# Kernel tuning notes

Measured on AMD Instinct MI355X. Metric: run time of the kernel, lower is better.

Reference implementation:

```python
import jax, jax.numpy as jnp
import numpy as np

INPUT_DIM, HIDDEN_DIM, OUTPUT_DIM = 512, 1024, 512
BATCH, SEQ = 64, 512


def setup_inputs() -> dict:
    key = jax.random.key(0)
    ks = jax.random.split(key, 7)
    s_ih = 1.0 / np.sqrt(HIDDEN_DIM)
    x = jax.random.normal(ks[0], (BATCH, SEQ, INPUT_DIM), dtype=jnp.float32)
    W_ih = jax.random.uniform(ks[1], (HIDDEN_DIM, INPUT_DIM), jnp.float32, -s_ih, s_ih)
    W_hh = jax.random.uniform(ks[2], (HIDDEN_DIM, HIDDEN_DIM), jnp.float32, -s_ih, s_ih)
    b_ih = jax.random.uniform(ks[3], (HIDDEN_DIM,), jnp.float32, -s_ih, s_ih)
    b_hh = jax.random.uniform(ks[4], (HIDDEN_DIM,), jnp.float32, -s_ih, s_ih)
    s_fc = 1.0 / np.sqrt(HIDDEN_DIM)
    W_fc = jax.random.uniform(ks[5], (OUTPUT_DIM, HIDDEN_DIM), jnp.float32, -s_fc, s_fc)
    b_fc = jax.random.uniform(ks[6], (OUTPUT_DIM,), jnp.float32, -s_fc, s_fc)
    return {"x": x, "W_ih": W_ih, "W_hh": W_hh, "b_ih": b_ih,
            "b_hh": b_hh, "W_fc": W_fc, "b_fc": b_fc}


def reference(x, W_ih, W_hh, b_ih, b_hh, W_fc, b_fc):
    B = x.shape[0]
    # Precompute input projections for all timesteps in one big GEMM: [S, B, H]
    xp = jnp.einsum('bsi,hi->sbh', x, W_ih) + b_ih + b_hh

    def step(h, xp_t):
        h_new = jnp.tanh(xp_t + h @ W_hh.T)
        return h_new, None

    h0 = jnp.zeros((B, W_hh.shape[0]), dtype=x.dtype)
    h_final, _ = jax.lax.scan(step, h0, xp)
    return h_final @ W_fc.T + b_fc
```

## Files before the change

kernel.cpp:

```cpp
#include <hip/hip_runtime.h>
#include <hip/hip_fp16.h>

typedef _Float16 f16;
typedef _Float16 half8 __attribute__((ext_vector_type(8)));
typedef _Float16 half4 __attribute__((ext_vector_type(4)));
typedef float f32x4_t __attribute__((ext_vector_type(4)));
typedef unsigned int uint;
typedef unsigned int uint32x4 __attribute__((ext_vector_type(4)));

#define IN_DIM 512
#define H_DIM 1024
#define OUT_DIM 512
#define NBATCH 64
#define NSEQ 512
#define NGROUP 4
#define MB 16
#define WPG 16
#define NJ 64

__global__ __launch_bounds__(256) void cvt_f32_f16_k(const float* __restrict__ src,
                                                     f16* __restrict__ dst, int n) {
  int i = (blockIdx.x * 256 + threadIdx.x) * 4;
  if (i + 3 < n) {
    float4 v = *(const float4*)(src + i);
    half4 h;
    h[0] = (f16)v.x; h[1] = (f16)v.y; h[2] = (f16)v.z; h[3] = (f16)v.w;
    *(half4*)(dst + i) = h;
  }
}

__global__ __launch_bounds__(256) void bias_sum_k(const float* __restrict__ a,
                                                  const float* __restrict__ b,
                                                  float* __restrict__ o) {
  int i = blockIdx.x * 256 + threadIdx.x;
  if (i < H_DIM) o[i] = a[i] + b[i];
}

__global__ __launch_bounds__(256) void xp_gemm_k(
    const float* __restrict__ x, const float* __restrict__ wih,
    const float* __restrict__ bsum, f16* __restrict__ xp2)
{
  __shared__ f16 Alds[128 * 32];
  __shared__ f16 Blds[128 * 32];
  const int tid = threadIdx.x;
  const int l = tid & 63;
  const int w = tid >> 6;
  const int r0 = blockIdx.x * 128;
  const int n0 = blockIdx.y * 128;
  const int wm = (w >> 1) << 6;
  const int wn = (w & 1) << 6;
  const int srow = tid >> 1;
  const int scol = (tid & 1) << 4;
  const float* ax = x   + (size_t)(r0 + srow) * IN_DIM + scol;
  const float* bw = wih + (size_t)(n0 + srow) * IN_DIM + scol;
  const uint swz  = (uint)(srow & 7) << 4;
  const uint soff = (uint)srow * 64 + (uint)(tid & 1) * 32;
  char* Ab = (char*)Alds;
  char* Bb = (char*)Blds;

  f32x4_t acc[4][4];
  f32x4_t zv; zv[0] = 0.f; zv[1] = 0.f; zv[2] = 0.f; zv[3] = 0.f;
#pragma unroll
  for (int i = 0; i < 4; ++i)
#pragma unroll
    for (int j = 0; j < 4; ++j) acc[i][j] = zv;

  for (int k0 = 0; k0 < IN_DIM; k0 += 32) {
    float4 a0 = *(const float4*)(ax + k0);
    float4 a1 = *(const float4*)(ax + k0 + 4);
    float4 a2 = *(const float4*)(ax + k0 + 8);
    float4 a3 = *(const float4*)(ax + k0 + 12);
    float4 c0 = *(const float4*)(bw + k0);
    float4 c1 = *(const float4*)(bw + k0 + 4);
    float4 c2 = *(const float4*)(bw + k0 + 8);
    float4 c3 = *(const float4*)(bw + k0 + 12);
    __syncthreads();
    half8 pa0, pa1, pb0, pb1;
    pa0[0]=(f16)a0.x; pa0[1]=(f16)a0.y; pa0[2]=(f16)a0.z; pa0[3]=(f16)a0.w;
    pa0[4]=(f16)a1.x; pa0[5]=(f16)a1.y; pa0[6]=(f16)a1.z; pa0[7]=(f16)a1.w;
    pa1[0]=(f16)a2.x; pa1[1]=(f16)a2.y; pa1[2]=(f16)a2.z; pa1[3]=(f16)a2.w;
    pa1[4]=(f16)a3.x; pa1[5]=(f16)a3.y; pa1[6]=(f16)a3.z; pa1[7]=(f16)a3.w;
    pb0[0]=(f16)c0.x; pb0[1]=(f16)c0.y; pb0[2]=(f16)c0.z; pb0[3]=(f16)c0.w;
    pb0[4]=(f16)c1.x; pb0[5]=(f16)c1.y; pb0[6]=(f16)c1.z; pb0[7]=(f16)c1.w;
    pb1[0]=(f16)c2.x; pb1[1]=(f16)c2.y; pb1[2]=(f16)c2.z; pb1[3]=(f16)c2.w;
    pb1[4]=(f16)c3.x; pb1[5]=(f16)c3.y; pb1[6]=(f16)c3.z; pb1[7]=(f16)c3.w;
    *(half8*)(Ab + (soff ^ swz)) = pa0;
    *(half8*)(Ab + ((soff + 16) ^ swz)) = pa1;
    *(half8*)(Bb + (soff ^ swz)) = pb0;
    *(half8*)(Bb + ((soff + 16) ^ swz)) = pb1;
    __syncthreads();
    half8 af[4], bf[4];
#pragma unroll
    for (int mt = 0; mt < 4; ++mt) {
      uint rr = (uint)(wm + mt * 16 + (l & 15));
      uint off = rr * 64 + ((uint)(l >> 4) << 4);
      af[mt] = *(const half8*)(Ab + (off ^ ((rr & 7) << 4)));
    }
#pragma unroll
    for (int nt = 0; nt < 4; ++nt) {
      uint rr = (uint)(wn + nt * 16 + (l & 15));
      uint off = rr * 64 + ((uint)(l >> 4) << 4);
      bf[nt] = *(const half8*)(Bb + (off ^ ((rr & 7) << 4)));
    }
#pragma unroll
    for (int mt = 0; mt < 4; ++mt)
#pragma unroll
      for (int nt = 0; nt < 4; ++nt)
        acc[mt][nt] = __builtin_amdgcn_mfma_f32_16x16x32_f16(af[mt], bf[nt], acc[mt][nt], 0, 0, 0);
  }

#pragma unroll
  for (int nt = 0; nt < 4; ++nt) {
    const int n = n0 + wn + nt * 16 + (l & 15);
    const float bv = bsum[n];
#pragma unroll
    for (int mt = 0; mt < 4; ++mt) {
#pragma unroll
      for (int i = 0; i < 4; ++i) {
        int r = r0 + wm + mt * 16 + ((l >> 4) << 2) + i;
        int s = r & (NSEQ - 1);
        int b = r >> 9;
        xp2[((size_t)s * NBATCH + b) * H_DIM + n] = (f16)(acc[mt][nt][i] + bv);
      }
    }
  }
}

__global__ __launch_bounds__(256) void rnn_scan_k(
    const f16* __restrict__ whh2, const f16* __restrict__ xp2,
    f16* __restrict__ hbuf, uint* __restrict__ flags)
{
  __shared__ f16 hlds[MB * H_DIM];
  const int tid = threadIdx.x;
  const int l   = tid & 63;
  const int w   = tid >> 6;
  const int bid = blockIdx.x;
  const int xcd = bid & 7;
  const int g    = xcd >> 1;
  const int slot = ((bid >> 3) << 1) | (xcd & 1);
  const int j0   = slot * NJ + w * 16;
  const int c     = l & 15;
  const int brow0 = (l >> 4) << 2;

  half8 wf[32];
  {
    const f16* wp = whh2 + (size_t)(j0 + c) * H_DIM + ((l >> 4) << 3);
#pragma unroll
    for (int kt = 0; kt < 32; ++kt) wf[kt] = *(const half8*)(wp + kt * 32);
  }

  f16* hb0 = hbuf + (size_t)g * (2 * MB * H_DIM);
  uint* gflags = flags + g * 64;
  const int myflag = slot * 4 + w;
  const uint roff = (uint)c * 2048 + ((uint)(l >> 4) << 4);
  const uint rswz = ((uint)c & 7) << 4;
  char* hldsc = (char*)hlds;

  for (int t = 0; t < NSEQ; ++t) {
    const f16* hcur = hb0 + (t & 1) * (MB * H_DIM);
    uint* hnxt32 = (uint*)(hb0 + ((t + 1) & 1) * (MB * H_DIM));

    const f16* xpb = xp2 + ((size_t)t * NBATCH + g * MB + brow0) * H_DIM + (j0 + c);
    f16 x0 = xpb[0];
    f16 x1 = xpb[H_DIM];
    f16 x2 = xpb[2 * H_DIM];
    f16 x3 = xpb[3 * H_DIM];

    f32x4_t acc;
    acc[0] = (float)x0; acc[1] = (float)x1; acc[2] = (float)x2; acc[3] = (float)x3;

    if (t > 0) {
      if (w == 0) {
        while (true) {
          uint v = __hip_atomic_load(&gflags[l], __ATOMIC_RELAXED, __HIP_MEMORY_SCOPE_AGENT);
          if (__all((int)(v >= (uint)t))) break;
        }
      }
      __syncthreads();

      uint32x4 sv[8];
#pragma unroll
      for (int q = 0; q < 8; ++q) {
        const char* p = (const char*)hcur + (size_t)(q * 256 + tid) * 16;
        asm volatile("global_load_dwordx4 %0, %1, off sc0 sc1"
                     : "=v"(sv[q]) : "v"(p) : "memory");
      }
      asm volatile("s_waitcnt vmcnt(0)" ::: "memory");
      __builtin_amdgcn_sched_barrier(0);
#pragma unroll
      for (int q = 0; q < 8; ++q) {
        uint boff = (uint)(q * 256 + tid) * 16;
        uint row = boff >> 11;
        *(uint32x4*)(hldsc + (boff ^ ((row & 7) << 4))) = sv[q];
      }
      __syncthreads();

#pragma unroll
      for (int kt = 0; kt < 32; ++kt) {
        half8 af = *(const half8*)(hldsc + ((roff + (uint)kt * 64) ^ rswz));
        acc = __builtin_amdgcn_mfma_f32_16x16x32_f16(af, wf[kt], acc, 0, 0, 0);
      }
    }

    uint st[4];
#pragma unroll
    for (int i = 0; i < 4; ++i) {
      float pre = acc[i];
      float e = __expf(2.0f * pre);
      float th = 1.0f - 2.0f / (e + 1.0f);
      f16 hf = (f16)th;
      uint myv = (uint)__builtin_bit_cast(unsigned short, hf);
      uint pv = __shfl_xor(myv, 1, 64);
      st[i] = myv | (pv << 16);
    }
    if ((c & 1) == 0) {
#pragma unroll
      for (int i = 0; i < 4; ++i) {
        uint idx = (uint)(brow0 + i) * 512 + (uint)((j0 + c) >> 1);
        __hip_atomic_store(hnxt32 + idx, st[i], __ATOMIC_RELAXED, __HIP_MEMORY_SCOPE_AGENT);
      }
    }
    asm volatile("s_waitcnt vmcnt(0)" ::: "memory");
    if (l == 0) {
      __hip_atomic_store(&gflags[myflag], (uint)(t + 1), __ATOMIC_RELAXED, __HIP_MEMORY_SCOPE_AGENT);
    }
  }
}

__global__ __launch_bounds__(64) void fc_out_k(
    const f16* __restrict__ hbuf, const f16* __restrict__ wfc2,
    const float* __restrict__ bfc, float* __restrict__ out)
{
  const int l = threadIdx.x;
  const int wg = blockIdx.x;
  const int m0 = wg & 3;
  const int n0 = (wg >> 2) << 4;
  const f16* ap = hbuf + (size_t)m0 * (2 * MB * H_DIM)
                  + (size_t)(l & 15) * H_DIM + ((l >> 4) << 3);
  const f16* bp = wfc2 + (size_t)(n0 + (l & 15)) * H_DIM + ((l >> 4) << 3);
  f32x4_t acc;
  float bv = bfc[n0 + (l & 15)];
  acc[0] = bv; acc[1] = bv; acc[2] = bv; acc[3] = bv;
#pragma unroll
  for (int kt = 0; kt < 32; ++kt) {
    half8 a = *(const half8*)(ap + kt * 32);
    half8 b = *(const half8*)(bp + kt * 32);
    acc = __builtin_amdgcn_mfma_f32_16x16x32_f16(a, b, acc, 0, 0, 0);
  }
  const int b0 = (m0 << 4) + ((l >> 4) << 2);
  const int o  = n0 + (l & 15);
#pragma unroll
  for (int i = 0; i < 4; ++i) out[(size_t)(b0 + i) * OUT_DIM + o] = acc[i];
}

extern "C" void kernel_launch(void* const* d_in, const int* in_sizes, int n_in,
                              void* d_out, int out_size, void* d_ws, size_t ws_size,
                              hipStream_t stream) {
  const float* x   = (const float*)d_in[0];
  const float* wih = (const float*)d_in[1];
  const float* whh = (const float*)d_in[2];
  const float* bih = (const float*)d_in[3];
  const float* bhh = (const float*)d_in[4];
  const float* wfc = (const float*)d_in[5];
  const float* bfc = (const float*)d_in[6];
  float* out = (float*)d_out;
  char* ws = (char*)d_ws;

  f16*   xp2  = (f16*)(ws);
  f16*   whh2 = (f16*)(ws + (size_t)(64 << 20));
  f16*   wfc2 = (f16*)(ws + (size_t)(66 << 20));
  float* bsum = (float*)(ws + (size_t)(67 << 20));
  f16*   hbuf = (f16*)(ws + (size_t)(67 << 20) + 65536);
  uint*  flags= (uint*)(ws + (size_t)(67 << 20) + 65536 + 262144);

  hipMemsetAsync(flags, 0, 1024, stream);

  hipLaunchKernelGGL(cvt_f32_f16_k, dim3(1024), dim3(256), 0, stream, whh, whh2, H_DIM * H_DIM);
  hipLaunchKernelGGL(cvt_f32_f16_k, dim3(512),  dim3(256), 0, stream, wfc, wfc2, OUT_DIM * H_DIM);
  hipLaunchKernelGGL(bias_sum_k,    dim3(4),    dim3(256), 0, stream, bih, bhh, bsum);
  hipLaunchKernelGGL(xp_gemm_k,     dim3(256, 8), dim3(256), 0, stream, x, wih, bsum, xp2);
  hipLaunchKernelGGL(rnn_scan_k,    dim3(64),   dim3(256), 0, stream, whh2, xp2, hbuf, flags);
  hipLaunchKernelGGL(fc_out_k,      dim3(128),  dim3(64),  0, stream, hbuf, wfc2, bfc, out);
}
```

Before: 1.631 ms.

## Replace LDS staging in RNN scan with parity-tagged ring buffer direct loads

The recurrent scan no longer stages h through shared memory with two block barriers per step. Each wave now polls the flags and loads its MFMA A-fragments directly from a 32-slot ring buffer in global memory. A parity bit stored in the low mantissa bit of every f16 h value lets readers check that the data is complete and retry if not, so the producer no longer waits on its data stores before raising its flag. The MMA chain is also split into four independent accumulators to add instruction-level parallelism. The costs are 4x more L2 reads per block per step, possible reload spins, and a perturbed LSB in every hidden-state value.

```diff
diff --git a/kernel.cpp b/kernel.cpp
--- a/kernel.cpp
+++ b/kernel.cpp
@@ -17,6 +17,7 @@
 #define MB 16
 #define WPG 16
 #define NJ 64
+#define RING 32
 
 __global__ __launch_bounds__(256) void cvt_f32_f16_k(const float* __restrict__ src,
                                                      f16* __restrict__ dst, int n) {
@@ -34,6 +35,13 @@
                                                   float* __restrict__ o) {
   int i = blockIdx.x * 256 + threadIdx.x;
   if (i < H_DIM) o[i] = a[i] + b[i];
+}
+
+__global__ __launch_bounds__(256) void fill_pat_k(uint32x4* __restrict__ p, int n4) {
+  int i = blockIdx.x * 256 + threadIdx.x;
+  uint32x4 v;
+  v[0] = 0x0001FFFEu; v[1] = 0x0001FFFEu; v[2] = 0x0001FFFEu; v[3] = 0x0001FFFEu;
+  if (i < n4) p[i] = v;
 }
 
 __global__ __launch_bounds__(256) void xp_gemm_k(
@@ -126,11 +134,10 @@
   }
 }
 
-__global__ __launch_bounds__(256) void rnn_scan_k(
+__global__ __launch_bounds__(256, 1) void rnn_scan_k(
     const f16* __restrict__ whh2, const f16* __restrict__ xp2,
     f16* __restrict__ hbuf, uint* __restrict__ flags)
 {
-  __shared__ f16 hlds[MB * H_DIM];
   const int tid = threadIdx.x;
   const int l   = tid & 63;
   const int w   = tid >> 6;
@@ -149,81 +156,86 @@
     for (int kt = 0; kt < 32; ++kt) wf[kt] = *(const half8*)(wp + kt * 32);
   }
 
-  f16* hb0 = hbuf + (size_t)g * (2 * MB * H_DIM);
+  f16* gbase = hbuf + (size_t)g * (RING * MB * H_DIM);
   uint* gflags = flags + g * 64;
   const int myflag = slot * 4 + w;
-  const uint roff = (uint)c * 2048 + ((uint)(l >> 4) << 4);
-  const uint rswz = ((uint)c & 7) << 4;
-  char* hldsc = (char*)hlds;
+  const uint frag_off = (uint)c * (H_DIM * 2) + ((uint)(l >> 4) << 4);
 
   for (int t = 0; t < NSEQ; ++t) {
-    const f16* hcur = hb0 + (t & 1) * (MB * H_DIM);
-    uint* hnxt32 = (uint*)(hb0 + ((t + 1) & 1) * (MB * H_DIM));
-
     const f16* xpb = xp2 + ((size_t)t * NBATCH + g * MB + brow0) * H_DIM + (j0 + c);
     f16 x0 = xpb[0];
     f16 x1 = xpb[H_DIM];
     f16 x2 = xpb[2 * H_DIM];
     f16 x3 = xpb[3 * H_DIM];
 
-    f32x4_t acc;
-    acc[0] = (float)x0; acc[1] = (float)x1; acc[2] = (float)x2; acc[3] = (float)x3;
+    f32x4_t acc0, acc1, acc2, acc3;
+    acc0[0] = (float)x0; acc0[1] = (float)x1; acc0[2] = (float)x2; acc0[3] = (float)x3;
+#pragma unroll
+    for (int i = 0; i < 4; ++i) { acc1[i] = 0.f; acc2[i] = 0.f; acc3[i] = 0.f; }
 
     if (t > 0) {
-      if (w == 0) {
-        while (true) {
-          uint v = __hip_atomic_load(&gflags[l], __ATOMIC_RELAXED, __HIP_MEMORY_SCOPE_AGENT);
-          if (__all((int)(v >= (uint)t))) break;
+      while (true) {
+        uint v = __hip_atomic_load(&gflags[l], __ATOMIC_RELAXED, __HIP_MEMORY_SCOPE_AGENT);
+        if (__all((int)(v >= (uint)t))) break;
+      }
+      const char* sbase = (const char*)gbase
+                        + (size_t)(t & (RING - 1)) * (MB * H_DIM * 2) + frag_off;
+      const uint pexp = ((t >> 5) & 1) ? 0x00010001u : 0u;
+      uint32x4 sv[32];
+      for (;;) {
+#pragma unroll
+        for (int kt = 0; kt < 32; ++kt)
+          asm volatile("global_load_dwordx4 %0, %1, off offset:%2 sc0 sc1"
+                       : "=v"(sv[kt]) : "v"(sbase), "i"(kt * 64) : "memory");
+        asm volatile("s_waitcnt vmcnt(0)" ::: "memory");
+        uint bad;
+        if (pexp) {
+          uint a = 0xFFFFFFFFu;
+#pragma unroll
+          for (int kt = 0; kt < 32; ++kt) a &= sv[kt][0] & sv[kt][1] & sv[kt][2] & sv[kt][3];
+          bad = ~a & 0x00010001u;
+        } else {
+          uint o = 0u;
+#pragma unroll
+          for (int kt = 0; kt < 32; ++kt) o |= sv[kt][0] | sv[kt][1] | sv[kt][2] | sv[kt][3];
+          bad = o & 0x00010001u;
         }
-      }
-      __syncthreads();
-
-      uint32x4 sv[8];
-#pragma unroll
-      for (int q = 0; q < 8; ++q) {
-        const char* p = (const char*)hcur + (size_t)(q * 256 + tid) * 16;
-        asm volatile("global_load_dwordx4 %0, %1, off sc0 sc1"
-                     : "=v"(sv[q]) : "v"(p) : "memory");
-      }
-      asm volatile("s_waitcnt vmcnt(0)" ::: "memory");
-      __builtin_amdgcn_sched_barrier(0);
-#pragma unroll
-      for (int q = 0; q < 8; ++q) {
-        uint boff = (uint)(q * 256 + tid) * 16;
-        uint row = boff >> 11;
-        *(uint32x4*)(hldsc + (boff ^ ((row & 7) << 4))) = sv[q];
-      }
-      __syncthreads();
-
-#pragma unroll
-      for (int kt = 0; kt < 32; ++kt) {
-        half8 af = *(const half8*)(hldsc + ((roff + (uint)kt * 64) ^ rswz));
-        acc = __builtin_amdgcn_mfma_f32_16x16x32_f16(af, wf[kt], acc, 0, 0, 0);
-      }
-    }
-
+        if (!__any((int)(bad != 0u))) break;
+      }
+#pragma unroll
+      for (int kt = 0; kt < 32; kt += 4) {
+        acc0 = __builtin_amdgcn_mfma_f32_16x16x32_f16(__builtin_bit_cast(half8, sv[kt + 0]), wf[kt + 0], acc0, 0, 0, 0);
+        acc1 = __builtin_amdgcn_mfma_f32_16x16x32_f16(__builtin_bit_cast(half8, sv[kt + 1]), wf[kt + 1], acc1, 0, 0, 0);
+        acc2 = __builtin_amdgcn_mfma_f32_16x16x32_f16(__builtin_bit_cast(half8, sv[kt + 2]), wf[kt + 2], acc2, 0, 0, 0);
+        acc3 = __builtin_amdgcn_mfma_f32_16x16x32_f16(__builtin_bit_cast(half8, sv[kt + 3]), wf[kt + 3], acc3, 0, 0, 0);
+      }
+    }
+
+    f32x4_t accs = (acc0 + acc1) + (acc2 + acc3);
+
+    const uint pnew = (((t + 1) >> 5) & 1) ? 1u : 0u;
     uint st[4];
 #pragma unroll
     for (int i = 0; i < 4; ++i) {
-      float pre = acc[i];
+      float pre = accs[i];
       float e = __expf(2.0f * pre);
       float th = 1.0f - 2.0f / (e + 1.0f);
       f16 hf = (f16)th;
-      uint myv = (uint)__builtin_bit_cast(unsigned short, hf);
-      uint pv = __shfl_xor(myv, 1, 64);
-      st[i] = myv | (pv << 16);
-    }
+      uint hb = (uint)__builtin_bit_cast(unsigned short, hf);
+      hb = (hb & 0xFFFEu) | pnew;
+      uint pv = __shfl_xor(hb, 1, 64);
+      st[i] = hb | (pv << 16);
+    }
+    uint* nb = (uint*)((char*)gbase + (size_t)((t + 1) & (RING - 1)) * (MB * H_DIM * 2));
     if ((c & 1) == 0) {
 #pragma unroll
       for (int i = 0; i < 4; ++i) {
-        uint idx = (uint)(brow0 + i) * 512 + (uint)((j0 + c) >> 1);
-        __hip_atomic_store(hnxt32 + idx, st[i], __ATOMIC_RELAXED, __HIP_MEMORY_SCOPE_AGENT);
-      }
-    }
-    asm volatile("s_waitcnt vmcnt(0)" ::: "memory");
-    if (l == 0) {
+        uint idx = (uint)(brow0 + i) * (H_DIM / 2) + (uint)((j0 + c) >> 1);
+        __hip_atomic_store(nb + idx, st[i], __ATOMIC_RELAXED, __HIP_MEMORY_SCOPE_AGENT);
+      }
+    }
+    if (l == 0)
       __hip_atomic_store(&gflags[myflag], (uint)(t + 1), __ATOMIC_RELAXED, __HIP_MEMORY_SCOPE_AGENT);
-    }
   }
 }
 
@@ -235,7 +247,7 @@
   const int wg = blockIdx.x;
   const int m0 = wg & 3;
   const int n0 = (wg >> 2) << 4;
-  const f16* ap = hbuf + (size_t)m0 * (2 * MB * H_DIM)
+  const f16* ap = hbuf + (size_t)m0 * (RING * MB * H_DIM)
                   + (size_t)(l & 15) * H_DIM + ((l >> 4) << 3);
   const f16* bp = wfc2 + (size_t)(n0 + (l & 15)) * H_DIM + ((l >> 4) << 3);
   f32x4_t acc;
@@ -271,9 +283,11 @@
   f16*   wfc2 = (f16*)(ws + (size_t)(66 << 20));
   float* bsum = (float*)(ws + (size_t)(67 << 20));
   f16*   hbuf = (f16*)(ws + (size_t)(67 << 20) + 65536);
-  uint*  flags= (uint*)(ws + (size_t)(67 << 20) + 65536 + 262144);
+  uint*  flags= (uint*)(ws + (size_t)(67 << 20) + 65536 + (4 << 20));
 
   hipMemsetAsync(flags, 0, 1024, stream);
+  hipLaunchKernelGGL(fill_pat_k, dim3(1024), dim3(256), 0, stream,
+                     (uint32x4*)hbuf, (4 << 20) / 16);
 
   hipLaunchKernelGGL(cvt_f32_f16_k, dim3(1024), dim3(256), 0, stream, whh, whh2, H_DIM * H_DIM);
   hipLaunchKernelGGL(cvt_f32_f16_k, dim3(512),  dim3(256), 0, stream, wfc, wfc2, OUT_DIM * H_DIM);
```

Result: slower. 3.142 ms (+92.7%).
